# Optimization experiments

Hardware: AMD Instinct MI355X
Metric: run time of the kernel (lower is better)

## Reference

```python
import jax, jax.numpy as jnp
import numpy as np

B, T, TEMP, H, M = 2048, 168, 128, 1024, 48


def lstm_cell(x, h, c, Wih, Whh, bih, bhh):
    # PyTorch gate order: i, f, g, o
    gates = x @ Wih.T + h @ Whh.T + bih + bhh  # [B, 4H]
    i, f, g, o = jnp.split(gates, 4, axis=-1)
    i = jax.nn.sigmoid(i)
    f = jax.nn.sigmoid(f)
    g = jnp.tanh(g)
    o = jax.nn.sigmoid(o)
    c_new = f * c + i * g
    h_new = o * jnp.tanh(c_new)
    return h_new, c_new


def setup_inputs() -> dict:
    key = jax.random.key(0)
    ks = jax.random.split(key, 12)
    s_e = 1.0 / np.sqrt(H)
    u = lambda k, shape: jax.random.uniform(k, shape, jnp.float32, -s_e, s_e)
    return {
        "temp_seq": jax.random.normal(ks[0], (B, T, TEMP), jnp.float32),
        "avg_speeds": jax.random.normal(ks[1], (B, M), jnp.float32),
        "enc_Wih": u(ks[2], (4 * H, TEMP)),
        "enc_Whh": u(ks[3], (4 * H, H)),
        "enc_bih": u(ks[4], (4 * H,)),
        "enc_bhh": u(ks[5], (4 * H,)),
        "dec_Wih": u(ks[6], (4 * H, TEMP + 1)),
        "dec_Whh": u(ks[7], (4 * H, H)),
        "dec_bih": u(ks[8], (4 * H,)),
        "dec_bhh": u(ks[9], (4 * H,)),
        "fc_W": u(ks[10], (TEMP, H)),
        "fc_b": u(ks[11], (TEMP,)),
    }


def reference(temp_seq, avg_speeds, enc_Wih, enc_Whh, enc_bih, enc_bhh,
              dec_Wih, dec_Whh, dec_bih, dec_bhh, fc_W, fc_b):
    b = temp_seq.shape[0]
    h0 = jnp.zeros((b, H), temp_seq.dtype)
    c0 = jnp.zeros((b, H), temp_seq.dtype)

    # Encoder: LSTM over time, keep only final (h, c)
    def enc_step(carry, x_t):
        h, c = carry
        h, c = lstm_cell(x_t, h, c, enc_Wih, enc_Whh, enc_bih, enc_bhh)
        return (h, c), None

    (h_n, c_n), _ = jax.lax.scan(enc_step, (h0, c0), jnp.swapaxes(temp_seq, 0, 1))

    input_temp0 = temp_seq[:, -1, :]  # [B, TEMP]

    def dec_step(carry, speed_t):
        h, c, x_temp = carry
        x = jnp.concatenate([x_temp, speed_t[:, None]], axis=-1)  # [B, TEMP+1]
        h, c = lstm_cell(x, h, c, dec_Wih, dec_Whh, dec_bih, dec_bhh)
        pred = h @ fc_W.T + fc_b  # [B, TEMP]
        return (h, c, pred), pred

    _, preds = jax.lax.scan(dec_step, (h_n, c_n, input_temp0),
                            jnp.swapaxes(avg_speeds, 0, 1))
    return jnp.swapaxes(preds, 0, 1)  # [B, M, TEMP]
```

## Files before the change

kernel.cpp:

```cpp
#include <hip/hip_runtime.h>
#include <stdint.h>

#define B_SZ   2048
#define T_ENC  168
#define TEMPD  128
#define HID    1024
#define M_DEC  48

typedef _Float16 f16;
typedef _Float16 half8 __attribute__((ext_vector_type(8)));
typedef float    f32x4 __attribute__((ext_vector_type(4)));

__device__ __forceinline__ float sigf(float x)   { return 1.0f / (1.0f + __expf(-x)); }
__device__ __forceinline__ float tanhf_(float x) { return 2.0f / (1.0f + __expf(-2.0f * x)) - 1.0f; }

__device__ __forceinline__ void gld16(const void* g, void* l) {
    __builtin_amdgcn_global_load_lds(
        (const __attribute__((address_space(1))) void*)g,
        (__attribute__((address_space(3))) void*)l, 16, 0, 0);
}

__global__ void prep_misc(
    const float* __restrict__ encWih, const float* __restrict__ encWhh,
    const float* __restrict__ encbih, const float* __restrict__ encbhh,
    const float* __restrict__ decWih, const float* __restrict__ decWhh,
    const float* __restrict__ decbih, const float* __restrict__ decbhh,
    const float* __restrict__ fcW,    const float* __restrict__ temp_seq,
    f16* __restrict__ Wenc, f16* __restrict__ Wdec0, f16* __restrict__ fcWh,
    float* __restrict__ enc_b, float* __restrict__ dec_b,
    float* __restrict__ wlast, f16* __restrict__ x_temp)
{
    const int NW = 4 * HID * (TEMPD + HID);
    for (int idx = blockIdx.x * blockDim.x + threadIdx.x; idx < NW;
         idx += gridDim.x * blockDim.x) {
        int j = idx / (TEMPD + HID);
        int k = idx - j * (TEMPD + HID);
        Wenc[idx]  = (f16)(k < TEMPD ? encWih[j * TEMPD + k]
                                     : encWhh[(size_t)j * HID + (k - TEMPD)]);
        Wdec0[idx] = (f16)(k < TEMPD ? decWih[j * (TEMPD + 1) + k]
                                     : decWhh[(size_t)j * HID + (k - TEMPD)]);
        if (idx < TEMPD * HID) fcWh[idx] = (f16)fcW[idx];
        if (idx < 4 * HID) {
            enc_b[idx] = encbih[idx] + encbhh[idx];
            dec_b[idx] = decbih[idx] + decbhh[idx];
            wlast[idx] = decWih[idx * (TEMPD + 1) + TEMPD];
        }
        if (idx < B_SZ * TEMPD) {
            int b = idx >> 7, kk = idx & 127;
            x_temp[idx] = (f16)temp_seq[(size_t)b * (T_ENC * TEMPD) + (T_ENC - 1) * TEMPD + kk];
        }
    }
}

__global__ void prep_fold(
    const float* __restrict__ decWih, const float* __restrict__ decWhh,
    const float* __restrict__ decbih, const float* __restrict__ decbhh,
    const float* __restrict__ fcW,    const float* __restrict__ fcb,
    f16* __restrict__ WdecF, float* __restrict__ biasF)
{
    __shared__ float wih[TEMPD];
    const int j = blockIdx.x;
    const int k = blockIdx.y * 256 + threadIdx.x;
    if (threadIdx.x < TEMPD) wih[threadIdx.x] = decWih[j * (TEMPD + 1) + threadIdx.x];
    __syncthreads();
    float acc = decWhh[(size_t)j * HID + k];
    #pragma unroll 8
    for (int p = 0; p < TEMPD; ++p) acc += wih[p] * fcW[p * HID + k];
    WdecF[(size_t)j * HID + k] = (f16)acc;
    if (blockIdx.y == 0 && threadIdx.x == 0) {
        float b = decbih[j] + decbhh[j];
        for (int p = 0; p < TEMPD; ++p) b += wih[p] * fcb[p];
        biasF[j] = b;
    }
}

template <int MODE>
__global__ __launch_bounds__(512, 2)
void lstm_step(
    const void* __restrict__ xsrc, int xoff,
    const f16* __restrict__ h_in, f16* __restrict__ h_out, float* __restrict__ c,
    const f16* __restrict__ W,
    const float* __restrict__ bias,
    const float* __restrict__ wlast, const float* __restrict__ speeds, int m_step)
{
    constexpr int NKC = (MODE == 2) ? 16 : 18;
    constexpr int WS  = (MODE == 2) ? HID : (HID + TEMPD);

    __shared__ half8 ldsA[2][1024];
    __shared__ half8 ldsW[2][2048];

    const int tid  = threadIdx.x;
    const int id   = blockIdx.x;
    const int swzb = (id & 7) * 32 + (id >> 3);
    const int bm   = swzb & 15;
    const int bn   = swzb >> 4;
    const int lane = tid & 63;
    const int wid  = tid >> 6;
    const int wr   = wid >> 2;
    const int wc   = wid & 3;

    f32x4 acc[4][4];
    #pragma unroll
    for (int g = 0; g < 4; ++g)
        #pragma unroll
        for (int mr = 0; mr < 4; ++mr)
            acc[g][mr] = (f32x4){0.f, 0.f, 0.f, 0.f};

    auto stage = [&](int b, int kc) {
        if (MODE == 0 && kc < 2) {
            const float* xs = (const float*)xsrc;
            #pragma unroll
            for (int it = 0; it < 2; ++it) {
                int chunk = tid + it * 512;
                int row = chunk >> 3, slot = chunk & 7;
                const float* p = xs + (size_t)(bm * 128 + row) * (T_ENC * TEMPD) + xoff + kc * 64 + slot * 8;
                float4 f0 = ((const float4*)p)[0];
                float4 f1 = ((const float4*)p)[1];
                union { uint4 u; f16 h[8]; } cv;
                cv.h[0] = (f16)f0.x; cv.h[1] = (f16)f0.y; cv.h[2] = (f16)f0.z; cv.h[3] = (f16)f0.w;
                cv.h[4] = (f16)f1.x; cv.h[5] = (f16)f1.y; cv.h[6] = (f16)f1.z; cv.h[7] = (f16)f1.w;
                *(uint4*)&ldsA[b][row * 8 + (slot ^ (row & 7))] = cv.u;
            }
        } else if (MODE == 1 && kc < 2) {
            const f16* xs = (const f16*)xsrc;
            #pragma unroll
            for (int it = 0; it < 2; ++it) {
                int p = wid * 128 + it * 64 + lane;
                int row = p >> 3, s = p & 7;
                gld16(xs + (size_t)(bm * 128 + row) * TEMPD + kc * 64 + ((s ^ (row & 7)) << 3),
                      &ldsA[b][wid * 128 + it * 64]);
            }
        } else {
            const int k0 = kc * 64 - (MODE == 2 ? 0 : TEMPD);
            #pragma unroll
            for (int it = 0; it < 2; ++it) {
                int p = wid * 128 + it * 64 + lane;
                int row = p >> 3, s = p & 7;
                gld16(h_in + (size_t)(bm * 128 + row) * HID + k0 + ((s ^ (row & 7)) << 3),
                      &ldsA[b][wid * 128 + it * 64]);
            }
        }
        {
            const int k0 = kc * 64;
            #pragma unroll
            for (int it = 0; it < 4; ++it) {
                int p = wid * 256 + it * 64 + lane;
                int r = p >> 3, s = p & 7;
                int g = r >> 6, j = r & 63;
                gld16(W + (size_t)(g * HID + bn * 64 + j) * WS + k0 + ((s ^ (r & 7)) << 3),
                      &ldsW[b][wid * 256 + it * 64]);
            }
        }
    };

    stage(0, 0);
    __syncthreads();

    int cur = 0;
    for (int kc = 0; kc < NKC; ++kc) {
        if (kc + 1 < NKC) stage(cur ^ 1, kc + 1);
        #pragma unroll
        for (int s = 0; s < 2; ++s) {
            const int ks = s * 4 + (lane >> 4);
            half8 af[4];
            #pragma unroll
            for (int mr = 0; mr < 4; ++mr) {
                int row = wr * 64 + mr * 16 + (lane & 15);
                af[mr] = ldsA[cur][row * 8 + (ks ^ (row & 7))];
            }
            half8 bf[4];
            #pragma unroll
            for (int g = 0; g < 4; ++g) {
                int r = g * 64 + wc * 16 + (lane & 15);
                bf[g] = ldsW[cur][r * 8 + (ks ^ (r & 7))];
            }
            __builtin_amdgcn_s_setprio(1);
            #pragma unroll
            for (int g = 0; g < 4; ++g)
                #pragma unroll
                for (int mr = 0; mr < 4; ++mr)
                    acc[g][mr] = __builtin_amdgcn_mfma_f32_16x16x32_f16(af[mr], bf[g], acc[g][mr], 0, 0, 0);
            __builtin_amdgcn_s_setprio(0);
        }
        __syncthreads();
        cur ^= 1;
    }

    const int col_g = bn * 64 + wc * 16 + (lane & 15);
    const float bi  = bias[col_g];
    const float bf_ = bias[HID + col_g];
    const float bg  = bias[2 * HID + col_g];
    const float bo  = bias[3 * HID + col_g];
    float wli = 0.f, wlf = 0.f, wlg = 0.f, wlo = 0.f;
    if (MODE >= 1) {
        wli = wlast[col_g];
        wlf = wlast[HID + col_g];
        wlg = wlast[2 * HID + col_g];
        wlo = wlast[3 * HID + col_g];
    }
    #pragma unroll
    for (int mr = 0; mr < 4; ++mr) {
        #pragma unroll
        for (int q = 0; q < 4; ++q) {
            int row_g = bm * 128 + wr * 64 + mr * 16 + (lane >> 4) * 4 + q;
            float pi = acc[0][mr][q] + bi;
            float pf = acc[1][mr][q] + bf_;
            float pg = acc[2][mr][q] + bg;
            float po = acc[3][mr][q] + bo;
            if (MODE >= 1) {
                float sp = speeds[(size_t)row_g * M_DEC + m_step];
                pi += sp * wli; pf += sp * wlf; pg += sp * wlg; po += sp * wlo;
            }
            float ii = sigf(pi), ff = sigf(pf), gg = tanhf_(pg), oo = sigf(po);
            size_t idx = (size_t)row_g * HID + col_g;
            float cn = ff * c[idx] + ii * gg;
            c[idx] = cn;
            h_out[idx] = (f16)(oo * tanhf_(cn));
        }
    }
}

__global__ __launch_bounds__(256, 2)
void fc_batch(const f16* __restrict__ hist, const f16* __restrict__ fcWh,
              const float* __restrict__ fcb, float* __restrict__ out, int mbase)
{
    __shared__ half8 ldsA[32 * 8];
    __shared__ half8 ldsW[128 * 8];
    const int tid  = threadIdx.x;
    const int lane = tid & 63;
    const int wid  = tid >> 6;
    const int wr   = wid >> 1;
    const int wc   = wid & 1;
    const int bm   = blockIdx.x;
    const int slot = bm >> 6;
    const int b0   = (bm & 63) * 32;
    const f16* hrow = hist + (size_t)slot * (B_SZ * HID) + (size_t)b0 * HID;
    const int  mm   = mbase + slot;

    f32x4 acc[4];
    #pragma unroll
    for (int nr = 0; nr < 4; ++nr) acc[nr] = (f32x4){0.f, 0.f, 0.f, 0.f};

    for (int kc = 0; kc < HID / 64; ++kc) {
        const int k0 = kc * 64;
        {
            int row = tid >> 3, s = tid & 7;
            gld16(hrow + (size_t)row * HID + k0 + ((s ^ (row & 7)) << 3), &ldsA[wid * 64]);
        }
        #pragma unroll
        for (int it = 0; it < 4; ++it) {
            int p = wid * 256 + it * 64 + lane;
            int row = p >> 3, s = p & 7;
            gld16(fcWh + (size_t)row * HID + k0 + ((s ^ (row & 7)) << 3), &ldsW[wid * 256 + it * 64]);
        }
        __syncthreads();
        #pragma unroll
        for (int s2 = 0; s2 < 2; ++s2) {
            int arow = wr * 16 + (lane & 15);
            int slotk = s2 * 4 + (lane >> 4);
            half8 a = ldsA[arow * 8 + (slotk ^ (arow & 7))];
            #pragma unroll
            for (int nr = 0; nr < 4; ++nr) {
                int brow = wc * 64 + nr * 16 + (lane & 15);
                half8 bfr = ldsW[brow * 8 + (slotk ^ (brow & 7))];
                acc[nr] = __builtin_amdgcn_mfma_f32_16x16x32_f16(a, bfr, acc[nr], 0, 0, 0);
            }
        }
        __syncthreads();
    }
    #pragma unroll
    for (int nr = 0; nr < 4; ++nr)
        #pragma unroll
        for (int q = 0; q < 4; ++q) {
            int rloc = wr * 16 + (lane >> 4) * 4 + q;
            int col  = wc * 64 + nr * 16 + (lane & 15);
            out[(size_t)(b0 + rloc) * (M_DEC * TEMPD) + (size_t)mm * TEMPD + col] = acc[nr][q] + fcb[col];
        }
}

extern "C" void kernel_launch(void* const* d_in, const int* in_sizes, int n_in,
                              void* d_out, int out_size, void* d_ws, size_t ws_size,
                              hipStream_t stream)
{
    (void)in_sizes; (void)n_in; (void)out_size; (void)ws_size;
    const float* temp_seq   = (const float*)d_in[0];
    const float* avg_speeds = (const float*)d_in[1];
    const float* enc_Wih    = (const float*)d_in[2];
    const float* enc_Whh    = (const float*)d_in[3];
    const float* enc_bih    = (const float*)d_in[4];
    const float* enc_bhh    = (const float*)d_in[5];
    const float* dec_Wih    = (const float*)d_in[6];
    const float* dec_Whh    = (const float*)d_in[7];
    const float* dec_bih    = (const float*)d_in[8];
    const float* dec_bhh    = (const float*)d_in[9];
    const float* fc_W       = (const float*)d_in[10];
    const float* fc_b       = (const float*)d_in[11];
    float* out = (float*)d_out;

    char* ws = (char*)d_ws;
    size_t off = 0;
    auto alloc = [&](size_t bytes) -> void* {
        void* p = ws + off;
        off += (bytes + 255) & ~(size_t)255;
        return p;
    };
    const size_t SLOT = (size_t)B_SZ * HID;
    f16*   Wenc   = (f16*)alloc((size_t)4 * HID * (TEMPD + HID) * 2);
    f16*   Wdec0  = (f16*)alloc((size_t)4 * HID * (TEMPD + HID) * 2);
    f16*   WdecF  = (f16*)alloc((size_t)4 * HID * HID * 2);
    f16*   fcWh   = (f16*)alloc((size_t)TEMPD * HID * 2);
    float* enc_b  = (float*)alloc((size_t)4 * HID * 4);
    float* dec_b  = (float*)alloc((size_t)4 * HID * 4);
    float* biasF  = (float*)alloc((size_t)4 * HID * 4);
    float* wlast  = (float*)alloc((size_t)4 * HID * 4);
    f16*   hA     = (f16*)alloc(SLOT * 2);
    f16*   hB     = (f16*)alloc(SLOT * 2);
    float* cbuf   = (float*)alloc(SLOT * 4);
    f16*   x_temp = (f16*)alloc((size_t)B_SZ * TEMPD * 2);
    f16*   hist   = (f16*)alloc(16 * SLOT * 2);

    hipMemsetAsync(hA,   0, SLOT * 2, stream);
    hipMemsetAsync(cbuf, 0, SLOT * 4, stream);

    prep_misc<<<8192, 256, 0, stream>>>(
        enc_Wih, enc_Whh, enc_bih, enc_bhh,
        dec_Wih, dec_Whh, dec_bih, dec_bhh,
        fc_W, temp_seq,
        Wenc, Wdec0, fcWh, enc_b, dec_b, wlast, x_temp);
    prep_fold<<<dim3(4096, 4), 256, 0, stream>>>(
        dec_Wih, dec_Whh, dec_bih, dec_bhh, fc_W, fc_b, WdecF, biasF);

    f16* hbuf[2] = {hA, hB};
    for (int t = 0; t < T_ENC; ++t) {
        lstm_step<0><<<256, 512, 0, stream>>>(
            (const void*)temp_seq, t * TEMPD,
            hbuf[t & 1], hbuf[(t + 1) & 1], cbuf,
            Wenc, enc_b, nullptr, nullptr, 0);
    }
    for (int m = 0; m < M_DEC; ++m) {
        const f16* hin = (m == 0) ? hA : hist + ((size_t)((m - 1) & 15)) * SLOT;
        f16* hout = hist + ((size_t)(m & 15)) * SLOT;
        if (m == 0) {
            lstm_step<1><<<256, 512, 0, stream>>>(
                (const void*)x_temp, 0, hin, hout, cbuf,
                Wdec0, dec_b, wlast, avg_speeds, 0);
        } else {
            lstm_step<2><<<256, 512, 0, stream>>>(
                nullptr, 0, hin, hout, cbuf,
                WdecF, biasF, wlast, avg_speeds, m);
        }
        if ((m & 15) == 15) {
            fc_batch<<<1024, 256, 0, stream>>>(hist, fcWh, fc_b, out, m - 15);
        }
    }
}
```

Before: 6.724 ms.

## Triple-buffer LSTM GEMM loads and pre-convert input sequence to fp16

```diff
diff --git a/kernel.cpp b/kernel.cpp
--- a/kernel.cpp
+++ b/kernel.cpp
@@ -20,15 +20,32 @@
         (__attribute__((address_space(3))) void*)l, 16, 0, 0);
 }
 
+#define WAITV6() asm volatile("s_waitcnt vmcnt(6)" ::: "memory")
+#define WAITV0() asm volatile("s_waitcnt vmcnt(0)" ::: "memory")
+#define SBAR()   do { __builtin_amdgcn_sched_barrier(0); \
+                      __builtin_amdgcn_s_barrier();      \
+                      __builtin_amdgcn_sched_barrier(0); } while (0)
+
+__global__ void prep_xseq(const float* __restrict__ temp_seq, f16* __restrict__ xseq)
+{
+    size_t i4 = ((size_t)blockIdx.x * blockDim.x + threadIdx.x) * 4;
+    size_t b  = i4 / (T_ENC * TEMPD);
+    size_t r  = i4 - b * (T_ENC * TEMPD);
+    size_t t  = r >> 7;
+    size_t d  = r & 127;
+    float4 v = *(const float4*)(temp_seq + i4);
+    f16* o = xseq + ((t * B_SZ) + b) * TEMPD + d;
+    o[0] = (f16)v.x; o[1] = (f16)v.y; o[2] = (f16)v.z; o[3] = (f16)v.w;
+}
+
 __global__ void prep_misc(
     const float* __restrict__ encWih, const float* __restrict__ encWhh,
+    const float* __restrict__ decWih, const float* __restrict__ decWhh,
     const float* __restrict__ encbih, const float* __restrict__ encbhh,
-    const float* __restrict__ decWih, const float* __restrict__ decWhh,
     const float* __restrict__ decbih, const float* __restrict__ decbhh,
-    const float* __restrict__ fcW,    const float* __restrict__ temp_seq,
+    const float* __restrict__ fcW,
     f16* __restrict__ Wenc, f16* __restrict__ Wdec0, f16* __restrict__ fcWh,
-    float* __restrict__ enc_b, float* __restrict__ dec_b,
-    float* __restrict__ wlast, f16* __restrict__ x_temp)
+    float* __restrict__ enc_b, float* __restrict__ dec_b, float* __restrict__ wlast)
 {
     const int NW = 4 * HID * (TEMPD + HID);
     for (int idx = blockIdx.x * blockDim.x + threadIdx.x; idx < NW;
@@ -45,49 +62,60 @@
             dec_b[idx] = decbih[idx] + decbhh[idx];
             wlast[idx] = decWih[idx * (TEMPD + 1) + TEMPD];
         }
-        if (idx < B_SZ * TEMPD) {
-            int b = idx >> 7, kk = idx & 127;
-            x_temp[idx] = (f16)temp_seq[(size_t)b * (T_ENC * TEMPD) + (T_ENC - 1) * TEMPD + kk];
-        }
-    }
-}
-
-__global__ void prep_fold(
+    }
+}
+
+__global__ __launch_bounds__(256)
+void prep_fold(
     const float* __restrict__ decWih, const float* __restrict__ decWhh,
     const float* __restrict__ decbih, const float* __restrict__ decbhh,
     const float* __restrict__ fcW,    const float* __restrict__ fcb,
     f16* __restrict__ WdecF, float* __restrict__ biasF)
 {
-    __shared__ float wih[TEMPD];
-    const int j = blockIdx.x;
-    const int k = blockIdx.y * 256 + threadIdx.x;
-    if (threadIdx.x < TEMPD) wih[threadIdx.x] = decWih[j * (TEMPD + 1) + threadIdx.x];
+    __shared__ float wih[16][TEMPD];
+    __shared__ float fcbL[TEMPD];
+    const int tid = threadIdx.x;
+    const int j0  = blockIdx.x * 16;
+    for (int i = tid; i < 16 * TEMPD; i += 256) {
+        int r = i >> 7, p = i & 127;
+        wih[r][p] = decWih[(size_t)(j0 + r) * (TEMPD + 1) + p];
+    }
+    if (tid < TEMPD) fcbL[tid] = fcb[tid];
     __syncthreads();
-    float acc = decWhh[(size_t)j * HID + k];
-    #pragma unroll 8
-    for (int p = 0; p < TEMPD; ++p) acc += wih[p] * fcW[p * HID + k];
-    WdecF[(size_t)j * HID + k] = (f16)acc;
-    if (blockIdx.y == 0 && threadIdx.x == 0) {
-        float b = decbih[j] + decbhh[j];
-        for (int p = 0; p < TEMPD; ++p) b += wih[p] * fcb[p];
-        biasF[j] = b;
-    }
-}
-
-template <int MODE>
+    for (int kk = 0; kk < 4; ++kk) {
+        int k = kk * 256 + tid;
+        float acc[16];
+        #pragma unroll
+        for (int r = 0; r < 16; ++r) acc[r] = decWhh[(size_t)(j0 + r) * HID + k];
+        for (int p = 0; p < TEMPD; ++p) {
+            float w = fcW[(size_t)p * HID + k];
+            #pragma unroll
+            for (int r = 0; r < 16; ++r) acc[r] += wih[r][p] * w;
+        }
+        #pragma unroll
+        for (int r = 0; r < 16; ++r) WdecF[(size_t)(j0 + r) * HID + k] = (f16)acc[r];
+    }
+    if (tid < 16) {
+        float b = decbih[j0 + tid] + decbhh[j0 + tid];
+        for (int p = 0; p < TEMPD; ++p) b += wih[tid][p] * fcbL[p];
+        biasF[j0 + tid] = b;
+    }
+}
+
+template <int FULLK, int DEC>
 __global__ __launch_bounds__(512, 2)
 void lstm_step(
-    const void* __restrict__ xsrc, int xoff,
+    const f16* __restrict__ xsrc,
     const f16* __restrict__ h_in, f16* __restrict__ h_out, float* __restrict__ c,
     const f16* __restrict__ W,
     const float* __restrict__ bias,
     const float* __restrict__ wlast, const float* __restrict__ speeds, int m_step)
 {
-    constexpr int NKC = (MODE == 2) ? 16 : 18;
-    constexpr int WS  = (MODE == 2) ? HID : (HID + TEMPD);
-
-    __shared__ half8 ldsA[2][1024];
-    __shared__ half8 ldsW[2][2048];
+    constexpr int NKC = FULLK ? 18 : 16;
+    constexpr int WS  = FULLK ? (HID + TEMPD) : HID;
+
+    __shared__ half8 ldsA[3][1024];
+    __shared__ half8 ldsW[3][2048];
 
     const int tid  = threadIdx.x;
     const int id   = blockIdx.x;
@@ -106,32 +134,17 @@
         for (int mr = 0; mr < 4; ++mr)
             acc[g][mr] = (f32x4){0.f, 0.f, 0.f, 0.f};
 
-    auto stage = [&](int b, int kc) {
-        if (MODE == 0 && kc < 2) {
-            const float* xs = (const float*)xsrc;
-            #pragma unroll
-            for (int it = 0; it < 2; ++it) {
-                int chunk = tid + it * 512;
-                int row = chunk >> 3, slot = chunk & 7;
-                const float* p = xs + (size_t)(bm * 128 + row) * (T_ENC * TEMPD) + xoff + kc * 64 + slot * 8;
-                float4 f0 = ((const float4*)p)[0];
-                float4 f1 = ((const float4*)p)[1];
-                union { uint4 u; f16 h[8]; } cv;
-                cv.h[0] = (f16)f0.x; cv.h[1] = (f16)f0.y; cv.h[2] = (f16)f0.z; cv.h[3] = (f16)f0.w;
-                cv.h[4] = (f16)f1.x; cv.h[5] = (f16)f1.y; cv.h[6] = (f16)f1.z; cv.h[7] = (f16)f1.w;
-                *(uint4*)&ldsA[b][row * 8 + (slot ^ (row & 7))] = cv.u;
-            }
-        } else if (MODE == 1 && kc < 2) {
-            const f16* xs = (const f16*)xsrc;
+    auto stageA = [&](int b, int kc) {
+        if (FULLK && kc < 2) {
             #pragma unroll
             for (int it = 0; it < 2; ++it) {
                 int p = wid * 128 + it * 64 + lane;
                 int row = p >> 3, s = p & 7;
-                gld16(xs + (size_t)(bm * 128 + row) * TEMPD + kc * 64 + ((s ^ (row & 7)) << 3),
+                gld16(xsrc + (size_t)(bm * 128 + row) * TEMPD + kc * 64 + ((s ^ (row & 7)) << 3),
                       &ldsA[b][wid * 128 + it * 64]);
             }
         } else {
-            const int k0 = kc * 64 - (MODE == 2 ? 0 : TEMPD);
+            const int k0 = kc * 64 - (FULLK ? TEMPD : 0);
             #pragma unroll
             for (int it = 0; it < 2; ++it) {
                 int p = wid * 128 + it * 64 + lane;
@@ -140,25 +153,31 @@
                       &ldsA[b][wid * 128 + it * 64]);
             }
         }
-        {
-            const int k0 = kc * 64;
-            #pragma unroll
-            for (int it = 0; it < 4; ++it) {
-                int p = wid * 256 + it * 64 + lane;
-                int r = p >> 3, s = p & 7;
-                int g = r >> 6, j = r & 63;
-                gld16(W + (size_t)(g * HID + bn * 64 + j) * WS + k0 + ((s ^ (r & 7)) << 3),
-                      &ldsW[b][wid * 256 + it * 64]);
-            }
-        }
     };
-
-    stage(0, 0);
-    __syncthreads();
+    auto stageW = [&](int b, int kc) {
+        const int k0 = kc * 64;
+        #pragma unroll
+        for (int it = 0; it < 4; ++it) {
+            int p = wid * 256 + it * 64 + lane;
+            int r = p >> 3, s = p & 7;
+            int g = r >> 6, j = r & 63;
+            gld16(W + (size_t)(g * HID + bn * 64 + j) * WS + k0 + ((s ^ (r & 7)) << 3),
+                  &ldsW[b][wid * 256 + it * 64]);
+        }
+    };
+
+    stageA(0, 0); stageW(0, 0);
+    stageA(1, 1); stageW(1, 1);
 
     int cur = 0;
     for (int kc = 0; kc < NKC; ++kc) {
-        if (kc + 1 < NKC) stage(cur ^ 1, kc + 1);
+        if (kc == NKC - 1) { WAITV0(); } else { WAITV6(); }
+        SBAR();
+        if (kc + 2 < NKC) {
+            int nb = cur + 2; if (nb >= 3) nb -= 3;
+            stageA(nb, kc + 2);
+            stageW(nb, kc + 2);
+        }
         #pragma unroll
         for (int s = 0; s < 2; ++s) {
             const int ks = s * 4 + (lane >> 4);
@@ -182,8 +201,7 @@
                     acc[g][mr] = __builtin_amdgcn_mfma_f32_16x16x32_f16(af[mr], bf[g], acc[g][mr], 0, 0, 0);
             __builtin_amdgcn_s_setprio(0);
         }
-        __syncthreads();
-        cur ^= 1;
+        cur = (cur == 2) ? 0 : cur + 1;
     }
 
     const int col_g = bn * 64 + wc * 16 + (lane & 15);
@@ -192,7 +210,7 @@
     const float bg  = bias[2 * HID + col_g];
     const float bo  = bias[3 * HID + col_g];
     float wli = 0.f, wlf = 0.f, wlg = 0.f, wlo = 0.f;
-    if (MODE >= 1) {
+    if (DEC) {
         wli = wlast[col_g];
         wlf = wlast[HID + col_g];
         wlg = wlast[2 * HID + col_g];
@@ -207,7 +225,7 @@
             float pf = acc[1][mr][q] + bf_;
             float pg = acc[2][mr][q] + bg;
             float po = acc[3][mr][q] + bo;
-            if (MODE >= 1) {
+            if (DEC) {
                 float sp = speeds[(size_t)row_g * M_DEC + m_step];
                 pi += sp * wli; pf += sp * wlf; pg += sp * wlg; po += sp * wlo;
             }
@@ -316,24 +334,24 @@
     f16*   hA     = (f16*)alloc(SLOT * 2);
     f16*   hB     = (f16*)alloc(SLOT * 2);
     float* cbuf   = (float*)alloc(SLOT * 4);
-    f16*   x_temp = (f16*)alloc((size_t)B_SZ * TEMPD * 2);
+    f16*   xseq   = (f16*)alloc((size_t)T_ENC * B_SZ * TEMPD * 2);
     f16*   hist   = (f16*)alloc(16 * SLOT * 2);
 
     hipMemsetAsync(hA,   0, SLOT * 2, stream);
     hipMemsetAsync(cbuf, 0, SLOT * 4, stream);
 
+    prep_xseq<<<(B_SZ * T_ENC * TEMPD / 4 + 255) / 256, 256, 0, stream>>>(temp_seq, xseq);
     prep_misc<<<8192, 256, 0, stream>>>(
-        enc_Wih, enc_Whh, enc_bih, enc_bhh,
-        dec_Wih, dec_Whh, dec_bih, dec_bhh,
-        fc_W, temp_seq,
-        Wenc, Wdec0, fcWh, enc_b, dec_b, wlast, x_temp);
-    prep_fold<<<dim3(4096, 4), 256, 0, stream>>>(
+        enc_Wih, enc_Whh, dec_Wih, dec_Whh,
+        enc_bih, enc_bhh, dec_bih, dec_bhh, fc_W,
+        Wenc, Wdec0, fcWh, enc_b, dec_b, wlast);
+    prep_fold<<<256, 256, 0, stream>>>(
         dec_Wih, dec_Whh, dec_bih, dec_bhh, fc_W, fc_b, WdecF, biasF);
 
     f16* hbuf[2] = {hA, hB};
     for (int t = 0; t < T_ENC; ++t) {
-        lstm_step<0><<<256, 512, 0, stream>>>(
-            (const void*)temp_seq, t * TEMPD,
+        lstm_step<1, 0><<<256, 512, 0, stream>>>(
+            xseq + (size_t)t * (B_SZ * TEMPD),
             hbuf[t & 1], hbuf[(t + 1) & 1], cbuf,
             Wenc, enc_b, nullptr, nullptr, 0);
     }
@@ -341,13 +359,12 @@
         const f16* hin = (m == 0) ? hA : hist + ((size_t)((m - 1) & 15)) * SLOT;
         f16* hout = hist + ((size_t)(m & 15)) * SLOT;
         if (m == 0) {
-            lstm_step<1><<<256, 512, 0, stream>>>(
-                (const void*)x_temp, 0, hin, hout, cbuf,
-                Wdec0, dec_b, wlast, avg_speeds, 0);
+            lstm_step<1, 1><<<256, 512, 0, stream>>>(
+                xseq + (size_t)(T_ENC - 1) * (B_SZ * TEMPD),
+                hin, hout, cbuf, Wdec0, dec_b, wlast, avg_speeds, 0);
         } else {
-            lstm_step<2><<<256, 512, 0, stream>>>(
-                nullptr, 0, hin, hout, cbuf,
-                WdecF, biasF, wlast, avg_speeds, m);
+            lstm_step<0, 1><<<256, 512, 0, stream>>>(
+                nullptr, hin, hout, cbuf, WdecF, biasF, wlast, avg_speeds, m);
         }
         if ((m & 15) == 15) {
             fc_batch<<<1024, 256, 0, stream>>>(hist, fcWh, fc_b, out, m - 15);
```

Result: no change. 6.821 ms (+1.4%).
